# Performance work log

Measured on AMD Instinct MI355X. Metric: run time of the kernel, lower is better.

## Reference

```python
import jax, jax.numpy as jnp
import numpy as np

EMBED_DIM = 512
HEAD_SIZE = 32
HEAD_DIM = 32  # constant used for scaling in the original code
B, T = 4, 4096


def setup_inputs() -> dict:
    key = jax.random.key(0)
    ks = jax.random.split(key, 9)
    s = 0.02
    return {
        "x": jax.random.normal(ks[0], (B, T, EMBED_DIM), dtype=jnp.float32),
        "Wq": jax.random.normal(ks[1], (EMBED_DIM, HEAD_SIZE), dtype=jnp.float32) * s,
        "bq": jnp.zeros((HEAD_SIZE,), dtype=jnp.float32),
        "Wk": jax.random.normal(ks[2], (EMBED_DIM, HEAD_SIZE), dtype=jnp.float32) * s,
        "bk": jnp.zeros((HEAD_SIZE,), dtype=jnp.float32),
        "Wv": jax.random.normal(ks[3], (EMBED_DIM, HEAD_SIZE), dtype=jnp.float32) * s,
        "bv": jnp.zeros((HEAD_SIZE,), dtype=jnp.float32),
        "Wp": jax.random.normal(ks[4], (HEAD_SIZE, EMBED_DIM), dtype=jnp.float32) * s,
        "bp": jnp.zeros((EMBED_DIM,), dtype=jnp.float32),
    }


def reference(x, Wq, bq, Wk, bk, Wv, bv, Wp, bp):
    # q, k, v: [B, T, head_size]
    q = x @ Wq + bq
    k = x @ Wk + bk
    v = x @ Wv + bv
    # scores: [B, T, T]
    scores = jnp.einsum("btd,bsd->bts", q, k) / jnp.sqrt(jnp.float32(HEAD_DIM))
    t = x.shape[1]
    causal = jnp.tril(jnp.ones((t, t), dtype=bool))  # lower-triangular incl. diag
    scores = jnp.where(causal, scores, jnp.float32(-1e9))
    weights = jax.nn.softmax(scores, axis=-1)
    attn = jnp.einsum("bts,bsd->btd", weights, v)  # [B, T, head_size]
    return attn @ Wp + bp  # [B, T, embed_dim]
```

## Files before the change

kernel.cpp:

```cpp
#include <hip/hip_runtime.h>
#include <hip/hip_bf16.h>

#define TSEQ   4096
#define NB     4
#define EMB    512
#define HS     32
#define NQ     16384

typedef float  f32x4  __attribute__((ext_vector_type(4)));
typedef __bf16 bf16x8 __attribute__((ext_vector_type(8)));
typedef __bf16 bf16x4 __attribute__((ext_vector_type(4)));

__global__ __launch_bounds__(128) void wt_pack(
    const float* __restrict__ Wq, const float* __restrict__ bq,
    const float* __restrict__ Wk, const float* __restrict__ bk,
    const float* __restrict__ Wv, const float* __restrict__ bv,
    const float* __restrict__ Wp,
    __bf16* __restrict__ wt, float* __restrict__ bsc,
    __bf16* __restrict__ wpt)
{
    if (blockIdx.x < 96) {
        const int c  = blockIdx.x;
        const int m  = c >> 5;
        const int cc = c & 31;
        const float* W    = (m == 0) ? Wq : (m == 1) ? Wk : Wv;
        const float* bias = (m == 0) ? bq : (m == 1) ? bk : bv;
        const float s     = (m == 0) ? 0.17677669529663687f : 1.0f;

        const int d0 = threadIdx.x * 4;
        bf16x4 o = { (__bf16)(W[(size_t)(d0 + 0) * HS + cc] * s),
                     (__bf16)(W[(size_t)(d0 + 1) * HS + cc] * s),
                     (__bf16)(W[(size_t)(d0 + 2) * HS + cc] * s),
                     (__bf16)(W[(size_t)(d0 + 3) * HS + cc] * s) };
        *(bf16x4*)(wt + (size_t)c * EMB + d0) = o;
        if (threadIdx.x == 0) bsc[c] = bias[cc] * s;
    } else {
        const int col = (blockIdx.x - 96) * 16 + (threadIdx.x >> 3);
        const int d0  = (threadIdx.x & 7) * 4;
        bf16x4 o = { (__bf16)Wp[(size_t)(d0 + 0) * EMB + col],
                     (__bf16)Wp[(size_t)(d0 + 1) * EMB + col],
                     (__bf16)Wp[(size_t)(d0 + 2) * EMB + col],
                     (__bf16)Wp[(size_t)(d0 + 3) * EMB + col] };
        *(bf16x4*)(wpt + (size_t)col * HS + d0) = o;
    }
}

__global__ __launch_bounds__(256) void qkv_mfma(
    const float* __restrict__ x,
    const __bf16* __restrict__ wt, const float* __restrict__ bsc,
    __bf16* __restrict__ qbf, __bf16* __restrict__ kbf, __bf16* __restrict__ vtb)
{
    const int tid  = threadIdx.x;
    const int lane = tid & 63;
    const int w    = tid >> 6;
    const int lr = lane & 15;
    const int lh = lane >> 4;
    const int tok0 = blockIdx.x * 16;
    const int k0   = w * 128;

    const float*  xp = x + (size_t)(tok0 + lr) * EMB + k0 + lh * 8;
    const __bf16* wp = wt + (size_t)lr * EMB + k0 + lh * 8;

    const f32x4 z = {0.f, 0.f, 0.f, 0.f};
    f32x4 acc[6] = {z, z, z, z, z, z};

    bf16x8 xf_c, wf_c[6], xf_n, wf_n[6];
    {
        const float4 a4 = *(const float4*)(xp);
        const float4 b4 = *(const float4*)(xp + 4);
        xf_c = bf16x8{ (__bf16)a4.x, (__bf16)a4.y, (__bf16)a4.z, (__bf16)a4.w,
                       (__bf16)b4.x, (__bf16)b4.y, (__bf16)b4.z, (__bf16)b4.w };
        #pragma unroll
        for (int f = 0; f < 6; ++f)
            wf_c[f] = *(const bf16x8*)(wp + (size_t)f * 16 * EMB);
    }

    #pragma unroll
    for (int kt = 0; kt < 128; kt += 32) {
        const int ktn = (kt + 32 < 128) ? (kt + 32) : kt;
        {
            const float4 a4 = *(const float4*)(xp + ktn);
            const float4 b4 = *(const float4*)(xp + ktn + 4);
            xf_n = bf16x8{ (__bf16)a4.x, (__bf16)a4.y, (__bf16)a4.z, (__bf16)a4.w,
                           (__bf16)b4.x, (__bf16)b4.y, (__bf16)b4.z, (__bf16)b4.w };
            #pragma unroll
            for (int f = 0; f < 6; ++f)
                wf_n[f] = *(const bf16x8*)(wp + (size_t)f * 16 * EMB + ktn);
        }

        acc[0] = __builtin_amdgcn_mfma_f32_16x16x32_bf16(wf_c[0], xf_c, acc[0], 0, 0, 0);
        acc[1] = __builtin_amdgcn_mfma_f32_16x16x32_bf16(wf_c[1], xf_c, acc[1], 0, 0, 0);
        acc[2] = __builtin_amdgcn_mfma_f32_16x16x32_bf16(wf_c[2], xf_c, acc[2], 0, 0, 0);
        acc[3] = __builtin_amdgcn_mfma_f32_16x16x32_bf16(wf_c[3], xf_c, acc[3], 0, 0, 0);
        acc[4] = __builtin_amdgcn_mfma_f32_16x16x32_bf16(xf_c, wf_c[4], acc[4], 0, 0, 0);
        acc[5] = __builtin_amdgcn_mfma_f32_16x16x32_bf16(xf_c, wf_c[5], acc[5], 0, 0, 0);

        xf_c = xf_n;
        #pragma unroll
        for (int f = 0; f < 6; ++f) wf_c[f] = wf_n[f];
    }

    __shared__ float red[3 * 6 * 256];
    if (w > 0) {
        #pragma unroll
        for (int i = 0; i < 6; ++i)
            *(f32x4*)&red[((w - 1) * 6 + i) * 256 + lane * 4] = acc[i];
    }
    __syncthreads();
    if (w != 0) return;

    #pragma unroll
    for (int i = 0; i < 6; ++i)
        #pragma unroll
        for (int ww = 0; ww < 3; ++ww)
            acc[i] += *(const f32x4*)&red[(ww * 6 + i) * 256 + lane * 4];

    #pragma unroll
    for (int f = 0; f < 2; ++f) {
        const int cb = f * 16 + lh * 4;
        const float4 bqv = *(const float4*)(bsc + cb);
        const float4 bkv = *(const float4*)(bsc + 32 + cb);
        bf16x4 oq = { (__bf16)(acc[f][0] + bqv.x), (__bf16)(acc[f][1] + bqv.y),
                      (__bf16)(acc[f][2] + bqv.z), (__bf16)(acc[f][3] + bqv.w) };
        bf16x4 ok = { (__bf16)(acc[2+f][0] + bkv.x), (__bf16)(acc[2+f][1] + bkv.y),
                      (__bf16)(acc[2+f][2] + bkv.z), (__bf16)(acc[2+f][3] + bkv.w) };
        *(bf16x4*)(qbf + (size_t)(tok0 + lr) * HS + cb) = oq;
        *(bf16x4*)(kbf + (size_t)(tok0 + lr) * HS + cb) = ok;
    }
    {
        const int b    = tok0 >> 12;
        const int t_in = (tok0 & (TSEQ - 1)) + lh * 4;
        #pragma unroll
        for (int f = 0; f < 2; ++f) {
            const int d = f * 16 + lr;
            const float bv1 = bsc[64 + d];
            bf16x4 o = { (__bf16)(acc[4+f][0] + bv1), (__bf16)(acc[4+f][1] + bv1),
                         (__bf16)(acc[4+f][2] + bv1), (__bf16)(acc[4+f][3] + bv1) };
            *(bf16x4*)(vtb + ((size_t)(b * HS + d)) * TSEQ + t_in) = o;
        }
    }
}

__device__ __forceinline__ void pstore(__bf16* Pb, int row, int col, float v) {
    const int c2 = (((col >> 3) ^ ((row >> 1) & 3)) << 3) | (col & 7);
    Pb[row * 32 + c2] = (__bf16)v;
}

__device__ __forceinline__ void s_stage(
    const bf16x8 qa0, const bf16x8 qa1,
    const bf16x8 ck0, const bf16x8 ck1,
    int kt, int q0, int lr, int lh,
    float lp[2][4], __bf16* Pb)
{
    const f32x4 z = {0.f, 0.f, 0.f, 0.f};
    f32x4 s00 = __builtin_amdgcn_mfma_f32_16x16x32_bf16(qa0, ck0, z, 0, 0, 0);
    f32x4 s01 = __builtin_amdgcn_mfma_f32_16x16x32_bf16(qa0, ck1, z, 0, 0, 0);
    f32x4 s10 = __builtin_amdgcn_mfma_f32_16x16x32_bf16(qa1, ck0, z, 0, 0, 0);
    f32x4 s11 = __builtin_amdgcn_mfma_f32_16x16x32_bf16(qa1, ck1, z, 0, 0, 0);

    float P[2][2][4];
    #pragma unroll
    for (int r = 0; r < 4; ++r) {
        P[0][0][r] = s00[r]; P[0][1][r] = s01[r];
        P[1][0][r] = s10[r]; P[1][1][r] = s11[r];
    }

    if (kt != q0) {
        #pragma unroll
        for (int qi = 0; qi < 2; ++qi)
            #pragma unroll
            for (int kj = 0; kj < 2; ++kj)
                #pragma unroll
                for (int r = 0; r < 4; ++r)
                    P[qi][kj][r] = __expf(P[qi][kj][r]);
    } else {
        #pragma unroll
        for (int qi = 0; qi < 2; ++qi)
            #pragma unroll
            for (int kj = 0; kj < 2; ++kj)
                #pragma unroll
                for (int r = 0; r < 4; ++r) {
                    const int qrow = qi * 16 + lh * 4 + r;
                    const int kcol = kj * 16 + lr;
                    P[qi][kj][r] = (kcol <= qrow) ? __expf(P[qi][kj][r]) : 0.f;
                }
    }

    #pragma unroll
    for (int qi = 0; qi < 2; ++qi)
        #pragma unroll
        for (int r = 0; r < 4; ++r)
            lp[qi][r] += P[qi][0][r] + P[qi][1][r];

    #pragma unroll
    for (int qi = 0; qi < 2; ++qi)
        #pragma unroll
        for (int kj = 0; kj < 2; ++kj)
            #pragma unroll
            for (int r = 0; r < 4; ++r)
                pstore(Pb, qi * 16 + lh * 4 + r, kj * 16 + lr, P[qi][kj][r]);
}

__device__ __forceinline__ void strip_proc(
    int kt0, int kend, int q0,
    const bf16x8 qa0, const bf16x8 qa1,
    const __bf16* kbase, const __bf16* vbase,
    __bf16* Pl,
    f32x4 o[4], float lp[2][4],
    int lr, int lh, int rd0, int rd1)
{
    if (kt0 >= kend) return;

    bf16x8 kf0 = *(const bf16x8*)(kbase + (size_t)kt0 * HS);
    bf16x8 kf1 = *(const bf16x8*)(kbase + (size_t)(kt0 + 16) * HS);
    bf16x8 vf0 = *(const bf16x8*)(vbase + kt0);
    bf16x8 vf1 = *(const bf16x8*)(vbase + kt0 + 16 * TSEQ);

    bf16x8 cv0p, cv1p;
    int pb = 1;
    {
        const bf16x8 ck0 = kf0, ck1 = kf1;
        cv0p = vf0; cv1p = vf1;
        const int ktn = (kt0 + 256 < kend) ? (kt0 + 256) : kt0;
        kf0 = *(const bf16x8*)(kbase + (size_t)ktn * HS);
        kf1 = *(const bf16x8*)(kbase + (size_t)(ktn + 16) * HS);
        vf0 = *(const bf16x8*)(vbase + ktn);
        vf1 = *(const bf16x8*)(vbase + ktn + 16 * TSEQ);
        s_stage(qa0, qa1, ck0, ck1, kt0, q0, lr, lh, lp, Pl);
    }

    for (int kt = kt0 + 256; kt < kend; kt += 256) {
        const bf16x8 ck0 = kf0, ck1 = kf1, cv0 = vf0, cv1 = vf1;
        const int ktn = (kt + 256 < kend) ? (kt + 256) : kt;
        kf0 = *(const bf16x8*)(kbase + (size_t)ktn * HS);
        kf1 = *(const bf16x8*)(kbase + (size_t)(ktn + 16) * HS);
        vf0 = *(const bf16x8*)(vbase + ktn);
        vf1 = *(const bf16x8*)(vbase + ktn + 16 * TSEQ);

        const __bf16* pbase = Pl + (pb ^ 1) * 1024;
        const bf16x8 pa0 = *(const bf16x8*)(pbase + rd0);
        const bf16x8 pa1 = *(const bf16x8*)(pbase + rd1);

        s_stage(qa0, qa1, ck0, ck1, kt, q0, lr, lh, lp, Pl + pb * 1024);

        o[0] = __builtin_amdgcn_mfma_f32_16x16x32_bf16(pa0, cv0p, o[0], 0, 0, 0);
        o[1] = __builtin_amdgcn_mfma_f32_16x16x32_bf16(pa0, cv1p, o[1], 0, 0, 0);
        o[2] = __builtin_amdgcn_mfma_f32_16x16x32_bf16(pa1, cv0p, o[2], 0, 0, 0);
        o[3] = __builtin_amdgcn_mfma_f32_16x16x32_bf16(pa1, cv1p, o[3], 0, 0, 0);

        cv0p = cv0; cv1p = cv1; pb ^= 1;
    }

    {
        const __bf16* pbase = Pl + (pb ^ 1) * 1024;
        const bf16x8 pa0 = *(const bf16x8*)(pbase + rd0);
        const bf16x8 pa1 = *(const bf16x8*)(pbase + rd1);
        o[0] = __builtin_amdgcn_mfma_f32_16x16x32_bf16(pa0, cv0p, o[0], 0, 0, 0);
        o[1] = __builtin_amdgcn_mfma_f32_16x16x32_bf16(pa0, cv1p, o[1], 0, 0, 0);
        o[2] = __builtin_amdgcn_mfma_f32_16x16x32_bf16(pa1, cv0p, o[2], 0, 0, 0);
        o[3] = __builtin_amdgcn_mfma_f32_16x16x32_bf16(pa1, cv1p, o[3], 0, 0, 0);
    }
}

__global__ __launch_bounds__(512) void attn_fused(
    const __bf16* __restrict__ qbf, const __bf16* __restrict__ kbf,
    const __bf16* __restrict__ vtb,
    const __bf16* __restrict__ wpt, const float* __restrict__ bp,
    float* __restrict__ out)
{
    const int p   = blockIdx.x;
    const int b   = blockIdx.y;
    const int tid = threadIdx.x;
    const int w    = tid >> 6;
    const int lane = tid & 63;
    const int lr = lane & 15;
    const int lh = lane >> 4;

    const int n0  = p + 1;
    const int q00 = p * 32;
    const int q01 = (127 - p) * 32;

    extern __shared__ char smem[];
    __bf16* Pl_all = (__bf16*)smem;
    float*  red    = (float*)smem;
    float*  lpred  = (float*)(smem + 65536);
    __bf16* attn_s = (__bf16*)(smem + 65536 + 2048);

    __bf16* myPl = Pl_all + w * 2048;

    const __bf16* qp0 = qbf + ((size_t)(b * TSEQ + q00 + lr)) * HS + lh * 8;
    const __bf16* qp1 = qbf + ((size_t)(b * TSEQ + q01 + lr)) * HS + lh * 8;
    const bf16x8 qa0s0 = *(const bf16x8*)qp0;
    const bf16x8 qa1s0 = *(const bf16x8*)(qp0 + 16 * HS);
    const bf16x8 qa0s1 = *(const bf16x8*)qp1;
    const bf16x8 qa1s1 = *(const bf16x8*)(qp1 + 16 * HS);

    const __bf16* kbase = kbf + ((size_t)(b * TSEQ + lr)) * HS + lh * 8;
    const __bf16* vbase = vtb + (size_t)(b * HS + lr) * TSEQ + lh * 8;

    const int swc = (lh ^ ((lr >> 1) & 3)) << 3;
    const int rd0 = lr * 32 + swc;
    const int rd1 = (16 + lr) * 32 + swc;

    const f32x4 z = {0.f, 0.f, 0.f, 0.f};
    f32x4 o0[4] = {z, z, z, z};
    f32x4 o1[4] = {z, z, z, z};
    float lp0[2][4] = {}, lp1[2][4] = {};

    strip_proc(w * 32, q00 + 32, q00, qa0s0, qa1s0, kbase, vbase, myPl,
               o0, lp0, lr, lh, rd0, rd1);
    const int tb = n0 + ((w - n0) & 7);
    strip_proc((tb - n0) * 32, q01 + 32, q01, qa0s1, qa1s1, kbase, vbase, myPl,
               o1, lp1, lr, lh, rd0, rd1);

    #pragma unroll
    for (int msk = 1; msk < 16; msk <<= 1) {
        #pragma unroll
        for (int qi = 0; qi < 2; ++qi)
            #pragma unroll
            for (int r = 0; r < 4; ++r) {
                lp0[qi][r] += __shfl_xor(lp0[qi][r], msk, 64);
                lp1[qi][r] += __shfl_xor(lp1[qi][r], msk, 64);
            }
    }

    __syncthreads();

    #pragma unroll
    for (int f = 0; f < 4; ++f) {
        *(f32x4*)&red[((w * 2 + 0) * 4 + f) * 256 + lane * 4] = o0[f];
        *(f32x4*)&red[((w * 2 + 1) * 4 + f) * 256 + lane * 4] = o1[f];
    }
    if (lr == 0) {
        #pragma unroll
        for (int qi = 0; qi < 2; ++qi)
            #pragma unroll
            for (int r = 0; r < 4; ++r) {
                lpred[(w * 2 + 0) * 32 + qi * 16 + lh * 4 + r] = lp0[qi][r];
                lpred[(w * 2 + 1) * 32 + qi * 16 + lh * 4 + r] = lp1[qi][r];
            }
    }
    __syncthreads();

    {
        const int s  = w >> 2;
        const int f  = w & 3;
        const int qh = f >> 1;
        const int dh = f & 1;
        f32x4 sum = z;
        #pragma unroll
        for (int ww = 0; ww < 8; ++ww)
            sum += *(const f32x4*)&red[((ww * 2 + s) * 4 + f) * 256 + lane * 4];

        #pragma unroll
        for (int r = 0; r < 4; ++r) {
            const int q = qh * 16 + lh * 4 + r;
            float L = 0.f;
            #pragma unroll
            for (int ww = 0; ww < 8; ++ww)
                L += lpred[(ww * 2 + s) * 32 + q];
            attn_s[(s * 32 + q) * 32 + dh * 16 + lr] = (__bf16)(sum[r] / L);
        }
    }
    __syncthreads();

    {
        const int sp = w >> 2;
        const int c0 = (w & 3) * 128;
        const int qb0 = (sp == 0) ? q00 : q01;
        const __bf16* as = attn_s + sp * 1024;
        const bf16x8 a0 = *(const bf16x8*)(as + lr * 32 + lh * 8);
        const bf16x8 a1 = *(const bf16x8*)(as + (16 + lr) * 32 + lh * 8);

        #pragma unroll
        for (int g = 0; g < 8; ++g) {
            const int c = c0 + g * 16;
            const bf16x8 wb = *(const bf16x8*)(wpt + (size_t)(c + lr) * HS + lh * 8);
            f32x4 d0 = __builtin_amdgcn_mfma_f32_16x16x32_bf16(a0, wb, z, 0, 0, 0);
            f32x4 d1 = __builtin_amdgcn_mfma_f32_16x16x32_bf16(a1, wb, z, 0, 0, 0);
            const float bpv = bp[c + lr];
            #pragma unroll
            for (int r = 0; r < 4; ++r) {
                const int row = lh * 4 + r;
                out[(size_t)(b * TSEQ + qb0 + row)      * EMB + c + lr] = d0[r] + bpv;
                out[(size_t)(b * TSEQ + qb0 + 16 + row) * EMB + c + lr] = d1[r] + bpv;
            }
        }
    }
}

extern "C" void kernel_launch(void* const* d_in, const int* in_sizes, int n_in,
                              void* d_out, int out_size, void* d_ws, size_t ws_size,
                              hipStream_t stream)
{
    const float* x  = (const float*)d_in[0];
    const float* Wq = (const float*)d_in[1];
    const float* bq = (const float*)d_in[2];
    const float* Wk = (const float*)d_in[3];
    const float* bk = (const float*)d_in[4];
    const float* Wv = (const float*)d_in[5];
    const float* bv = (const float*)d_in[6];
    const float* Wp = (const float*)d_in[7];
    const float* bp = (const float*)d_in[8];
    float* out = (float*)d_out;

    char* ws = (char*)d_ws;
    __bf16* wt  = (__bf16*)(ws);
    float*  bsc = (float*)(ws + 96 * 1024);
    __bf16* wpt = (__bf16*)(ws + 128 * 1024);
    __bf16* qbf = (__bf16*)(ws + (size_t)1 * 1024 * 1024);
    __bf16* kbf = (__bf16*)(ws + (size_t)2 * 1024 * 1024);
    __bf16* vtb = (__bf16*)(ws + (size_t)3 * 1024 * 1024);

    wt_pack<<<dim3(128), 128, 0, stream>>>(Wq, bq, Wk, bk, Wv, bv, Wp,
                                           wt, bsc, wpt);
    qkv_mfma<<<dim3(NQ / 16), 256, 0, stream>>>(x, wt, bsc, qbf, kbf, vtb);
    attn_fused<<<dim3(64, NB), 512, 71680, stream>>>(qbf, kbf, vtb, wpt, bp, out);
}
```

Before: 49.09 us.

## Compute transposed scores and give each block a single query tile

The score MFMA now computes S^T (keys as rows, queries as columns), so each lane holds four consecutive keys for one query. The P tile can then be written to LDS as packed bf16x4 stores with a 16-byte XOR swizzle instead of scalar swizzled stores, and the row-sum reduction needs only two shuffles. The grid goes from 64 blocks per batch, each pairing a short and a long causal strip, to 128 blocks that each own one 32-query tile. That drops the load-balancing pairing and its second strip, at the cost of uneven work across blocks and the epilogue reduction running on only half the waves.

```diff
diff --git a/kernel.cpp b/kernel.cpp
--- a/kernel.cpp
+++ b/kernel.cpp
@@ -141,73 +141,74 @@
     }
 }
 
-__device__ __forceinline__ void pstore(__bf16* Pb, int row, int col, float v) {
-    const int c2 = (((col >> 3) ^ ((row >> 1) & 3)) << 3) | (col & 7);
-    Pb[row * 32 + c2] = (__bf16)v;
-}
-
-__device__ __forceinline__ void s_stage(
-    const bf16x8 qa0, const bf16x8 qa1,
+__device__ __forceinline__ void s_stage2(
     const bf16x8 ck0, const bf16x8 ck1,
-    int kt, int q0, int lr, int lh,
-    float lp[2][4], __bf16* Pb)
+    const bf16x8 qb0, const bf16x8 qb1,
+    int kt, int q0, int lr, int lh, int swz,
+    float lp[2], char* Pb)
 {
     const f32x4 z = {0.f, 0.f, 0.f, 0.f};
-    f32x4 s00 = __builtin_amdgcn_mfma_f32_16x16x32_bf16(qa0, ck0, z, 0, 0, 0);
-    f32x4 s01 = __builtin_amdgcn_mfma_f32_16x16x32_bf16(qa0, ck1, z, 0, 0, 0);
-    f32x4 s10 = __builtin_amdgcn_mfma_f32_16x16x32_bf16(qa1, ck0, z, 0, 0, 0);
-    f32x4 s11 = __builtin_amdgcn_mfma_f32_16x16x32_bf16(qa1, ck1, z, 0, 0, 0);
+    f32x4 st00 = __builtin_amdgcn_mfma_f32_16x16x32_bf16(ck0, qb0, z, 0, 0, 0);
+    f32x4 st01 = __builtin_amdgcn_mfma_f32_16x16x32_bf16(ck1, qb0, z, 0, 0, 0);
+    f32x4 st10 = __builtin_amdgcn_mfma_f32_16x16x32_bf16(ck0, qb1, z, 0, 0, 0);
+    f32x4 st11 = __builtin_amdgcn_mfma_f32_16x16x32_bf16(ck1, qb1, z, 0, 0, 0);
 
     float P[2][2][4];
     #pragma unroll
     for (int r = 0; r < 4; ++r) {
-        P[0][0][r] = s00[r]; P[0][1][r] = s01[r];
-        P[1][0][r] = s10[r]; P[1][1][r] = s11[r];
+        P[0][0][r] = st00[r]; P[0][1][r] = st01[r];
+        P[1][0][r] = st10[r]; P[1][1][r] = st11[r];
     }
 
     if (kt != q0) {
         #pragma unroll
-        for (int qi = 0; qi < 2; ++qi)
-            #pragma unroll
-            for (int kj = 0; kj < 2; ++kj)
+        for (int qh = 0; qh < 2; ++qh)
+            #pragma unroll
+            for (int kh = 0; kh < 2; ++kh)
                 #pragma unroll
                 for (int r = 0; r < 4; ++r)
-                    P[qi][kj][r] = __expf(P[qi][kj][r]);
+                    P[qh][kh][r] = __expf(P[qh][kh][r]);
     } else {
         #pragma unroll
-        for (int qi = 0; qi < 2; ++qi)
-            #pragma unroll
-            for (int kj = 0; kj < 2; ++kj)
+        for (int qh = 0; qh < 2; ++qh)
+            #pragma unroll
+            for (int kh = 0; kh < 2; ++kh)
                 #pragma unroll
                 for (int r = 0; r < 4; ++r) {
-                    const int qrow = qi * 16 + lh * 4 + r;
-                    const int kcol = kj * 16 + lr;
-                    P[qi][kj][r] = (kcol <= qrow) ? __expf(P[qi][kj][r]) : 0.f;
+                    const int key_l = kh * 16 + lh * 4 + r;
+                    const int q_l   = qh * 16 + lr;
+                    P[qh][kh][r] = (key_l <= q_l) ? __expf(P[qh][kh][r]) : 0.f;
                 }
     }
 
     #pragma unroll
-    for (int qi = 0; qi < 2; ++qi)
-        #pragma unroll
-        for (int r = 0; r < 4; ++r)
-            lp[qi][r] += P[qi][0][r] + P[qi][1][r];
-
-    #pragma unroll
-    for (int qi = 0; qi < 2; ++qi)
-        #pragma unroll
-        for (int kj = 0; kj < 2; ++kj)
+    for (int qh = 0; qh < 2; ++qh) {
+        #pragma unroll
+        for (int kh = 0; kh < 2; ++kh)
             #pragma unroll
             for (int r = 0; r < 4; ++r)
-                pstore(Pb, qi * 16 + lh * 4 + r, kj * 16 + lr, P[qi][kj][r]);
-}
-
-__device__ __forceinline__ void strip_proc(
+                lp[qh] += P[qh][kh][r];
+    }
+
+    #pragma unroll
+    for (int qh = 0; qh < 2; ++qh)
+        #pragma unroll
+        for (int kh = 0; kh < 2; ++kh) {
+            const int q    = qh * 16 + lr;
+            const int byte = q * 128 + ((kh * 32 + lh * 8) ^ swz);
+            bf16x4 pk = { (__bf16)P[qh][kh][0], (__bf16)P[qh][kh][1],
+                          (__bf16)P[qh][kh][2], (__bf16)P[qh][kh][3] };
+            *(bf16x4*)(Pb + byte) = pk;
+        }
+}
+
+__device__ __forceinline__ void strip_proc2(
     int kt0, int kend, int q0,
-    const bf16x8 qa0, const bf16x8 qa1,
+    const bf16x8 qb0, const bf16x8 qb1,
     const __bf16* kbase, const __bf16* vbase,
-    __bf16* Pl,
-    f32x4 o[4], float lp[2][4],
-    int lr, int lh, int rd0, int rd1)
+    char* Pl,
+    f32x4 o[4], float lp[2],
+    int lr, int lh, int swz, int rdA, int rdB)
 {
     if (kt0 >= kend) return;
 
@@ -226,7 +227,7 @@
         kf1 = *(const bf16x8*)(kbase + (size_t)(ktn + 16) * HS);
         vf0 = *(const bf16x8*)(vbase + ktn);
         vf1 = *(const bf16x8*)(vbase + ktn + 16 * TSEQ);
-        s_stage(qa0, qa1, ck0, ck1, kt0, q0, lr, lh, lp, Pl);
+        s_stage2(ck0, ck1, qb0, qb1, kt0, q0, lr, lh, swz, lp, Pl);
     }
 
     for (int kt = kt0 + 256; kt < kend; kt += 256) {
@@ -237,11 +238,11 @@
         vf0 = *(const bf16x8*)(vbase + ktn);
         vf1 = *(const bf16x8*)(vbase + ktn + 16 * TSEQ);
 
-        const __bf16* pbase = Pl + (pb ^ 1) * 1024;
-        const bf16x8 pa0 = *(const bf16x8*)(pbase + rd0);
-        const bf16x8 pa1 = *(const bf16x8*)(pbase + rd1);
-
-        s_stage(qa0, qa1, ck0, ck1, kt, q0, lr, lh, lp, Pl + pb * 1024);
+        const char* pbase = Pl + (pb ^ 1) * 4096;
+        const bf16x8 pa0 = *(const bf16x8*)(pbase + rdA);
+        const bf16x8 pa1 = *(const bf16x8*)(pbase + rdB);
+
+        s_stage2(ck0, ck1, qb0, qb1, kt, q0, lr, lh, swz, lp, Pl + pb * 4096);
 
         o[0] = __builtin_amdgcn_mfma_f32_16x16x32_bf16(pa0, cv0p, o[0], 0, 0, 0);
         o[1] = __builtin_amdgcn_mfma_f32_16x16x32_bf16(pa0, cv1p, o[1], 0, 0, 0);
@@ -252,9 +253,9 @@
     }
 
     {
-        const __bf16* pbase = Pl + (pb ^ 1) * 1024;
-        const bf16x8 pa0 = *(const bf16x8*)(pbase + rd0);
-        const bf16x8 pa1 = *(const bf16x8*)(pbase + rd1);
+        const char* pbase = Pl + (pb ^ 1) * 4096;
+        const bf16x8 pa0 = *(const bf16x8*)(pbase + rdA);
+        const bf16x8 pa1 = *(const bf16x8*)(pbase + rdB);
         o[0] = __builtin_amdgcn_mfma_f32_16x16x32_bf16(pa0, cv0p, o[0], 0, 0, 0);
         o[1] = __builtin_amdgcn_mfma_f32_16x16x32_bf16(pa0, cv1p, o[1], 0, 0, 0);
         o[2] = __builtin_amdgcn_mfma_f32_16x16x32_bf16(pa1, cv0p, o[2], 0, 0, 0);
@@ -276,104 +277,75 @@
     const int lr = lane & 15;
     const int lh = lane >> 4;
 
-    const int n0  = p + 1;
-    const int q00 = p * 32;
-    const int q01 = (127 - p) * 32;
+    const int q0   = p * 32;
+    const int kend = q0 + 32;
 
     extern __shared__ char smem[];
-    __bf16* Pl_all = (__bf16*)smem;
+    char*   myPl   = smem + w * 8192;
     float*  red    = (float*)smem;
     float*  lpred  = (float*)(smem + 65536);
-    __bf16* attn_s = (__bf16*)(smem + 65536 + 2048);
-
-    __bf16* myPl = Pl_all + w * 2048;
-
-    const __bf16* qp0 = qbf + ((size_t)(b * TSEQ + q00 + lr)) * HS + lh * 8;
-    const __bf16* qp1 = qbf + ((size_t)(b * TSEQ + q01 + lr)) * HS + lh * 8;
-    const bf16x8 qa0s0 = *(const bf16x8*)qp0;
-    const bf16x8 qa1s0 = *(const bf16x8*)(qp0 + 16 * HS);
-    const bf16x8 qa0s1 = *(const bf16x8*)qp1;
-    const bf16x8 qa1s1 = *(const bf16x8*)(qp1 + 16 * HS);
+    __bf16* attn_s = (__bf16*)(smem + 65536 + 1024);
+
+    const __bf16* qp = qbf + ((size_t)(b * TSEQ + q0 + lr)) * HS + lh * 8;
+    const bf16x8 qb0 = *(const bf16x8*)qp;
+    const bf16x8 qb1 = *(const bf16x8*)(qp + 16 * HS);
 
     const __bf16* kbase = kbf + ((size_t)(b * TSEQ + lr)) * HS + lh * 8;
     const __bf16* vbase = vtb + (size_t)(b * HS + lr) * TSEQ + lh * 8;
 
-    const int swc = (lh ^ ((lr >> 1) & 3)) << 3;
-    const int rd0 = lr * 32 + swc;
-    const int rd1 = (16 + lr) * 32 + swc;
+    const int swz = (lr & 7) << 4;
+    const int rdA = lr * 128 + ((lh * 16) ^ swz);
+    const int rdB = (16 + lr) * 128 + ((lh * 16) ^ swz);
 
     const f32x4 z = {0.f, 0.f, 0.f, 0.f};
-    f32x4 o0[4] = {z, z, z, z};
-    f32x4 o1[4] = {z, z, z, z};
-    float lp0[2][4] = {}, lp1[2][4] = {};
-
-    strip_proc(w * 32, q00 + 32, q00, qa0s0, qa1s0, kbase, vbase, myPl,
-               o0, lp0, lr, lh, rd0, rd1);
-    const int tb = n0 + ((w - n0) & 7);
-    strip_proc((tb - n0) * 32, q01 + 32, q01, qa0s1, qa1s1, kbase, vbase, myPl,
-               o1, lp1, lr, lh, rd0, rd1);
-
-    #pragma unroll
-    for (int msk = 1; msk < 16; msk <<= 1) {
-        #pragma unroll
-        for (int qi = 0; qi < 2; ++qi)
-            #pragma unroll
-            for (int r = 0; r < 4; ++r) {
-                lp0[qi][r] += __shfl_xor(lp0[qi][r], msk, 64);
-                lp1[qi][r] += __shfl_xor(lp1[qi][r], msk, 64);
-            }
-    }
+    f32x4 o[4] = {z, z, z, z};
+    float lp[2] = {0.f, 0.f};
+
+    strip_proc2(w * 32, kend, q0, qb0, qb1, kbase, vbase, myPl,
+                o, lp, lr, lh, swz, rdA, rdB);
+
+    lp[0] += __shfl_xor(lp[0], 16, 64);
+    lp[0] += __shfl_xor(lp[0], 32, 64);
+    lp[1] += __shfl_xor(lp[1], 16, 64);
+    lp[1] += __shfl_xor(lp[1], 32, 64);
 
     __syncthreads();
 
     #pragma unroll
-    for (int f = 0; f < 4; ++f) {
-        *(f32x4*)&red[((w * 2 + 0) * 4 + f) * 256 + lane * 4] = o0[f];
-        *(f32x4*)&red[((w * 2 + 1) * 4 + f) * 256 + lane * 4] = o1[f];
-    }
-    if (lr == 0) {
-        #pragma unroll
-        for (int qi = 0; qi < 2; ++qi)
-            #pragma unroll
-            for (int r = 0; r < 4; ++r) {
-                lpred[(w * 2 + 0) * 32 + qi * 16 + lh * 4 + r] = lp0[qi][r];
-                lpred[(w * 2 + 1) * 32 + qi * 16 + lh * 4 + r] = lp1[qi][r];
-            }
+    for (int f = 0; f < 4; ++f)
+        *(f32x4*)&red[(w * 4 + f) * 256 + lane * 4] = o[f];
+    if (lh == 0) {
+        lpred[w * 32 + lr]      = lp[0];
+        lpred[w * 32 + 16 + lr] = lp[1];
     }
     __syncthreads();
 
-    {
-        const int s  = w >> 2;
-        const int f  = w & 3;
-        const int qh = f >> 1;
-        const int dh = f & 1;
+    if (w < 4) {
+        const int qh = w >> 1;
+        const int dh = w & 1;
         f32x4 sum = z;
         #pragma unroll
         for (int ww = 0; ww < 8; ++ww)
-            sum += *(const f32x4*)&red[((ww * 2 + s) * 4 + f) * 256 + lane * 4];
-
+            sum += *(const f32x4*)&red[(ww * 4 + w) * 256 + lane * 4];
         #pragma unroll
         for (int r = 0; r < 4; ++r) {
             const int q = qh * 16 + lh * 4 + r;
             float L = 0.f;
             #pragma unroll
             for (int ww = 0; ww < 8; ++ww)
-                L += lpred[(ww * 2 + s) * 32 + q];
-            attn_s[(s * 32 + q) * 32 + dh * 16 + lr] = (__bf16)(sum[r] / L);
+                L += lpred[ww * 32 + q];
+            attn_s[q * 32 + dh * 16 + lr] = (__bf16)(sum[r] / L);
         }
     }
     __syncthreads();
 
     {
-        const int sp = w >> 2;
-        const int c0 = (w & 3) * 128;
-        const int qb0 = (sp == 0) ? q00 : q01;
-        const __bf16* as = attn_s + sp * 1024;
-        const bf16x8 a0 = *(const bf16x8*)(as + lr * 32 + lh * 8);
-        const bf16x8 a1 = *(const bf16x8*)(as + (16 + lr) * 32 + lh * 8);
-
-        #pragma unroll
-        for (int g = 0; g < 8; ++g) {
+        const bf16x8 a0 = *(const bf16x8*)(attn_s + lr * 32 + lh * 8);
+        const bf16x8 a1 = *(const bf16x8*)(attn_s + (16 + lr) * 32 + lh * 8);
+        const int c0 = w * 64;
+
+        #pragma unroll
+        for (int g = 0; g < 4; ++g) {
             const int c = c0 + g * 16;
             const bf16x8 wb = *(const bf16x8*)(wpt + (size_t)(c + lr) * HS + lh * 8);
             f32x4 d0 = __builtin_amdgcn_mfma_f32_16x16x32_bf16(a0, wb, z, 0, 0, 0);
@@ -382,8 +354,8 @@
             #pragma unroll
             for (int r = 0; r < 4; ++r) {
                 const int row = lh * 4 + r;
-                out[(size_t)(b * TSEQ + qb0 + row)      * EMB + c + lr] = d0[r] + bpv;
-                out[(size_t)(b * TSEQ + qb0 + 16 + row) * EMB + c + lr] = d1[r] + bpv;
+                out[(size_t)(b * TSEQ + q0 + row)      * EMB + c + lr] = d0[r] + bpv;
+                out[(size_t)(b * TSEQ + q0 + 16 + row) * EMB + c + lr] = d1[r] + bpv;
             }
         }
     }
@@ -415,5 +387,5 @@
     wt_pack<<<dim3(128), 128, 0, stream>>>(Wq, bq, Wk, bk, Wv, bv, Wp,
                                            wt, bsc, wpt);
     qkv_mfma<<<dim3(NQ / 16), 256, 0, stream>>>(x, wt, bsc, qbf, kbf, vtb);
-    attn_fused<<<dim3(64, NB), 512, 71680, stream>>>(qbf, kbf, vtb, wpt, bp, out);
-}
+    attn_fused<<<dim3(128, NB), 512, 68608, stream>>>(qbf, kbf, vtb, wpt, bp, out);
+}
```

Measured after the change: 56.13 us. 14.4% more time.
